# Performance work log

Measured on AMD Instinct MI355X. Metric: run time of the kernel, lower is better.

The kernel has to match this reference:

```python
import jax, jax.numpy as jnp
import numpy as np

D = 64        # state dim (num_output)
H = 256       # MLP hidden width
B = 4096      # batch
NUM_STEPS = 16  # fixed-step Dormand-Prince steps over t in [0,1] per bijector


def _mlp(t, y, W1, b1, W2, b2, W3, b3):
    # time-conditioned MLP: concat scalar t to state, two tanh layers, linear out
    tcol = jnp.full((y.shape[0], 1), t, dtype=y.dtype)
    h = jnp.tanh(jnp.concatenate([y, tcol], axis=1) @ W1 + b1)
    h = jnp.tanh(h @ W2 + b2)
    return h @ W3 + b3


def _dopri5_fixed(f, y0):
    # classic Dormand-Prince (RK45) Butcher tableau, 5th-order solution,
    # fixed step h = 1/NUM_STEPS from t=0 to t=1
    h = jnp.asarray(1.0 / NUM_STEPS, dtype=y0.dtype)

    def step(y, i):
        t = i.astype(y0.dtype) * h
        k1 = f(t, y)
        k2 = f(t + h * (1/5),  y + h * ((1/5) * k1))
        k3 = f(t + h * (3/10), y + h * ((3/40) * k1 + (9/40) * k2))
        k4 = f(t + h * (4/5),  y + h * ((44/45) * k1 - (56/15) * k2 + (32/9) * k3))
        k5 = f(t + h * (8/9),  y + h * ((19372/6561) * k1 - (25360/2187) * k2
                                        + (64448/6561) * k3 - (212/729) * k4))
        k6 = f(t + h,          y + h * ((9017/3168) * k1 - (355/33) * k2
                                        + (46732/5247) * k3 + (49/176) * k4
                                        - (5103/18656) * k5))
        y_next = y + h * ((35/384) * k1 + (500/1113) * k3 + (125/192) * k4
                          - (2187/6784) * k5 + (11/84) * k6)
        return y_next, None

    y_final, _ = jax.lax.scan(step, y0, jnp.arange(NUM_STEPS))
    return y_final


def setup_inputs() -> dict:
    key = jax.random.key(0)
    ks = jax.random.split(key, 7)
    s_in = 1.0 / np.sqrt(D + 1)
    s_h = 1.0 / np.sqrt(H)
    inp = {"x": jax.random.normal(ks[0], (B, D), dtype=jnp.float32)}
    for i, base in enumerate([1, 4]):
        inp[f"p{i}_W1"] = jax.random.normal(ks[base], (D + 1, H), dtype=jnp.float32) * s_in
        inp[f"p{i}_b1"] = jnp.zeros((H,), dtype=jnp.float32)
        inp[f"p{i}_W2"] = jax.random.normal(ks[base + 1], (H, H), dtype=jnp.float32) * s_h
        inp[f"p{i}_b2"] = jnp.zeros((H,), dtype=jnp.float32)
        inp[f"p{i}_W3"] = jax.random.normal(ks[base + 2], (H, D), dtype=jnp.float32) * s_h
        inp[f"p{i}_b3"] = jnp.zeros((D,), dtype=jnp.float32)
    return inp


def reference(x, p0_W1, p0_b1, p0_W2, p0_b2, p0_W3, p0_b3,
              p1_W1, p1_b1, p1_W2, p1_b2, p1_W3, p1_b3):
    # Chain(list(reversed(bijectors))).forward applies bijector 0 first, then 1.
    # FFJORD bijector forward = integrate dz/dt = mlp(t, z) from t=0 to t=1.
    y = x
    params = [(p0_W1, p0_b1, p0_W2, p0_b2, p0_W3, p0_b3),
              (p1_W1, p1_b1, p1_W2, p1_b2, p1_W3, p1_b3)]
    for (W1, b1, W2, b2, W3, b3) in params:
        f = lambda t, z: _mlp(t, z, W1, b1, W2, b2, W3, b3)
        y = _dopri5_fixed(f, y)
    return y
```

## Files before the change

### kernel.cpp

```cpp
#include <hip/hip_runtime.h>

typedef __attribute__((ext_vector_type(8))) short short8;
typedef __attribute__((ext_vector_type(4))) float f32x4;

#define NSTEPS 16

__device__ __forceinline__ unsigned short bf16rne(float f) {
  unsigned int u = __float_as_uint(f);
  u += 0x7FFFu + ((u >> 16) & 1u);
  return (unsigned short)(u >> 16);
}

#if __has_builtin(__builtin_amdgcn_cvt_pk_bf16_f32)
typedef __attribute__((ext_vector_type(2))) __bf16 v2bf16;
__device__ __forceinline__ unsigned int pk2(float a, float b) {
  v2bf16 t = __builtin_amdgcn_cvt_pk_bf16_f32(a, b);
  unsigned int r;
  __builtin_memcpy(&r, &t, 4);
  return r;
}
#else
__device__ __forceinline__ unsigned int pk2(float a, float b) {
  unsigned int ua = __float_as_uint(a), ub = __float_as_uint(b);
  ua += 0x7FFFu + ((ua >> 16) & 1u);
  ub += 0x7FFFu + ((ub >> 16) & 1u);
  return (ua >> 16) | (ub & 0xFFFF0000u);
}
#endif

__device__ __forceinline__ float tanh_fast(float x) {
  float e = __builtin_amdgcn_exp2f(x * 2.8853900817779268f);
  return __builtin_fmaf(-2.0f, __builtin_amdgcn_rcpf(e + 1.0f), 1.0f);
}

__global__ void ffjord_setup(const float* __restrict__ W1a, const float* __restrict__ W2a,
                             const float* __restrict__ W3a, const float* __restrict__ W1b,
                             const float* __restrict__ W2b, const float* __restrict__ W3b,
                             unsigned short* __restrict__ ws) {
  int gid = blockIdx.x * blockDim.x + threadIdx.x;
  int bij = gid / 12288;
  int r = gid - bij * 12288;
  const float* W1 = bij ? W1b : W1a;
  const float* W2 = bij ? W2b : W2a;
  const float* W3 = bij ? W3b : W3a;
  unsigned short* o = ws + bij * 98304;
  const float* src;
  int kstride;
  if (r < 2048) {
    int lane = r & 63, nt = (r >> 6) & 15, ks = r >> 10;
    int k0 = ks * 32 + (lane >> 4) * 8, n = nt * 16 + (lane & 15);
    src = W1 + k0 * 256 + n; kstride = 256; o += r * 8;
  } else if (r < 10240) {
    int rr = r - 2048;
    int lane = rr & 63, nt = (rr >> 6) & 15, ks = rr >> 10;
    int k0 = ks * 32 + (lane >> 4) * 8, n = nt * 16 + (lane & 15);
    src = W2 + k0 * 256 + n; kstride = 256; o += 16384 + rr * 8;
  } else {
    int rr = r - 10240;
    int lane = rr & 63, nt = (rr >> 6) & 3, ks = rr >> 8;
    int k0 = ks * 32 + (lane >> 4) * 8, n = nt * 16 + (lane & 15);
    src = W3 + k0 * 64 + n; kstride = 64; o += 81920 + rr * 8;
  }
  #pragma unroll
  for (int j = 0; j < 8; j++) o[j] = bf16rne(src[j * kstride]);
}

__global__ __launch_bounds__(768, 3) void ffjord_main(
    const float* __restrict__ x, float* __restrict__ out,
    const unsigned short* __restrict__ ws,
    const float* __restrict__ W1a, const float* __restrict__ b1a,
    const float* __restrict__ b2a, const float* __restrict__ b3a,
    const float* __restrict__ W1b, const float* __restrict__ b1b,
    const float* __restrict__ b2b, const float* __restrict__ b3b) {
  __shared__ __align__(16) unsigned short zA[1088];
  __shared__ __align__(16) unsigned short h1A[4096];
  __shared__ __align__(16) unsigned short h2A[4096];
  __shared__ __align__(16) unsigned short w3s[16384];
  __shared__ __align__(16) float kbuf[5][1024];

  const int tid = threadIdx.x;
  const int wave = tid >> 6;
  const int lane = tid & 63;
  const int cl = lane & 15;
  const int qd = lane >> 4;
  const int row0 = blockIdx.x * 16;

  int hoff[2];
  #pragma unroll
  for (int t = 0; t < 2; t++) {
    int c = (wave * 2 + t) * 16 + qd * 4;
    hoff[t] = (c >> 5) * 512 + ((c & 31) >> 3) * 128 + cl * 8 + (c & 7);
  }
  const int zrb = qd * 136 + cl * 8;
  const int w3i = wave & 3;
  const int dl3 = w3i * 16 + qd * 4;
  const int zw = (2 * w3i + (qd >> 1)) * 136 + cl * 8 + 4 * (qd & 1);
  const int rtid = tid - 512;

  const float hstep = 1.0f / 16.0f;

  f32x4 yc;

  const float A2[5][5] = {
      {1.f / 5.f, 0.f, 0.f, 0.f, 0.f},
      {3.f / 40.f, 9.f / 40.f, 0.f, 0.f, 0.f},
      {44.f / 45.f, -56.f / 15.f, 32.f / 9.f, 0.f, 0.f},
      {19372.f / 6561.f, -25360.f / 2187.f, 64448.f / 6561.f, -212.f / 729.f, 0.f},
      {9017.f / 3168.f, -355.f / 33.f, 46732.f / 5247.f, 49.f / 176.f, -5103.f / 18656.f}};
  const float CT[6] = {0.0f, 0.2f, 0.3f, 0.8f, 8.0f / 9.0f, 1.0f};
  const float BW0 = 35.f / 384.f, BW2 = 500.f / 1113.f, BW3 = 125.f / 192.f,
              BW4 = -2187.f / 6784.f, BW5 = 11.f / 84.f;

  for (int bij = 0; bij < 2; bij++) {
    const unsigned short* wsb = ws + bij * 98304;
    const float* W1 = bij ? W1b : W1a;
    const float* b1 = bij ? b1b : b1a;
    const float* b2 = bij ? b2b : b2a;
    const float* b3 = bij ? b3b : b3a;

    f32x4 b1c[2], w1t4[2], b2c[2];
    short8 w1f[2][2], w2f[8][2];
    f32x4 b3c;

    if (wave < 8) {
      const short8* w1p = (const short8*)wsb;
      const short8* w2p = (const short8*)(wsb + 16384);
      #pragma unroll
      for (int t = 0; t < 2; t++) {
        int c = (wave * 2 + t) * 16 + qd * 4;
        b1c[t] = *(const f32x4*)(b1 + c);
        w1t4[t] = *(const f32x4*)(W1 + 64 * 256 + c);
        b2c[t] = *(const f32x4*)(b2 + c);
        #pragma unroll
        for (int ks = 0; ks < 2; ks++)
          w1f[ks][t] = w1p[(ks * 16 + wave * 2 + t) * 64 + lane];
        #pragma unroll
        for (int ks = 0; ks < 8; ks++)
          w2f[ks][t] = w2p[(ks * 16 + wave * 2 + t) * 64 + lane];
      }
    } else {
      b3c = *(const f32x4*)(b3 + dl3);
      if (bij == 0) {
        yc = *(const f32x4*)(x + (row0 + cl) * 64 + dl3);
        uint2 pv;
        pv.x = pk2(yc[0], yc[1]);
        pv.y = pk2(yc[2], yc[3]);
        *(uint2*)(zA + zw) = pv;
      }
    }

    {
      const uint4* s4 = (const uint4*)(wsb + 81920);
      uint4* d4 = (uint4*)w3s;
      for (int i = tid; i < 2048; i += 768) d4[i] = s4[i];
    }
    __syncthreads();

    for (int step = 0; step < NSTEPS; step++) {
      float stepf = (float)step;
      #pragma unroll
      for (int s = 0; s < 6; s++) {
        float ts = (stepf + CT[s]) * hstep;

        if (wave < 8) {
          short8 a0 = *(const short8*)(zA + zrb);
          short8 a1 = *(const short8*)(zA + zrb + 544);
          #pragma unroll
          for (int t = 0; t < 2; t++) {
            f32x4 acc;
            #pragma unroll
            for (int r = 0; r < 4; r++)
              acc[r] = __builtin_fmaf(ts, w1t4[t][r], b1c[t][r]);
            acc = __builtin_amdgcn_mfma_f32_16x16x32_bf16(w1f[0][t], a0, acc, 0, 0, 0);
            acc = __builtin_amdgcn_mfma_f32_16x16x32_bf16(w1f[1][t], a1, acc, 0, 0, 0);
            uint2 pv;
            pv.x = pk2(tanh_fast(acc[0]), tanh_fast(acc[1]));
            pv.y = pk2(tanh_fast(acc[2]), tanh_fast(acc[3]));
            *(uint2*)(h1A + hoff[t]) = pv;
          }
        }
        __syncthreads();

        if (wave < 8) {
          f32x4 a0A = b2c[0], a1A = b2c[1];
          f32x4 zf; zf[0] = 0.f; zf[1] = 0.f; zf[2] = 0.f; zf[3] = 0.f;
          f32x4 a0B = zf, a1B = zf;
          #pragma unroll
          for (int ks = 0; ks < 4; ks++) {
            short8 hb = ((const short8*)h1A)[ks * 64 + lane];
            a0A = __builtin_amdgcn_mfma_f32_16x16x32_bf16(w2f[ks][0], hb, a0A, 0, 0, 0);
            a1A = __builtin_amdgcn_mfma_f32_16x16x32_bf16(w2f[ks][1], hb, a1A, 0, 0, 0);
          }
          #pragma unroll
          for (int ks = 4; ks < 8; ks++) {
            short8 hb = ((const short8*)h1A)[ks * 64 + lane];
            a0B = __builtin_amdgcn_mfma_f32_16x16x32_bf16(w2f[ks][0], hb, a0B, 0, 0, 0);
            a1B = __builtin_amdgcn_mfma_f32_16x16x32_bf16(w2f[ks][1], hb, a1B, 0, 0, 0);
          }
          uint2 pv;
          pv.x = pk2(tanh_fast(a0A[0] + a0B[0]), tanh_fast(a0A[1] + a0B[1]));
          pv.y = pk2(tanh_fast(a0A[2] + a0B[2]), tanh_fast(a0A[3] + a0B[3]));
          *(uint2*)(h2A + hoff[0]) = pv;
          pv.x = pk2(tanh_fast(a1A[0] + a1B[0]), tanh_fast(a1A[1] + a1B[1]));
          pv.y = pk2(tanh_fast(a1A[2] + a1B[2]), tanh_fast(a1A[3] + a1B[3]));
          *(uint2*)(h2A + hoff[1]) = pv;
        }
        __syncthreads();

        if (wave >= 8) {
          f32x4 accP = b3c;
          f32x4 accQ; accQ[0] = 0.f; accQ[1] = 0.f; accQ[2] = 0.f; accQ[3] = 0.f;
          #pragma unroll
          for (int ks = 0; ks < 8; ks += 2) {
            short8 hb0 = ((const short8*)h2A)[ks * 64 + lane];
            short8 wf0 = ((const short8*)w3s)[(ks * 4 + w3i) * 64 + lane];
            short8 hb1 = ((const short8*)h2A)[(ks + 1) * 64 + lane];
            short8 wf1 = ((const short8*)w3s)[((ks + 1) * 4 + w3i) * 64 + lane];
            accP = __builtin_amdgcn_mfma_f32_16x16x32_bf16(wf0, hb0, accP, 0, 0, 0);
            accQ = __builtin_amdgcn_mfma_f32_16x16x32_bf16(wf1, hb1, accQ, 0, 0, 0);
          }
          f32x4 kc;
          #pragma unroll
          for (int r = 0; r < 4; r++) kc[r] = accP[r] + accQ[r];
          if (s < 5) *(f32x4*)(&kbuf[s][rtid * 4]) = kc;

          f32x4 z;
          if (s < 5) {
            #pragma unroll
            for (int r = 0; r < 4; r++)
              z[r] = __builtin_fmaf(hstep * A2[s][s], kc[r], yc[r]);
            #pragma unroll
            for (int j = 0; j < 4; j++)
              if (j < s) {
                f32x4 kj = *(const f32x4*)(&kbuf[j][rtid * 4]);
                float a = hstep * A2[s][j];
                #pragma unroll
                for (int r = 0; r < 4; r++) z[r] = __builtin_fmaf(a, kj[r], z[r]);
              }
          } else {
            f32x4 k0 = *(const f32x4*)(&kbuf[0][rtid * 4]);
            f32x4 k2 = *(const f32x4*)(&kbuf[2][rtid * 4]);
            f32x4 k3 = *(const f32x4*)(&kbuf[3][rtid * 4]);
            f32x4 k4 = *(const f32x4*)(&kbuf[4][rtid * 4]);
            #pragma unroll
            for (int r = 0; r < 4; r++) {
              float d = BW0 * k0[r] + BW2 * k2[r] + BW3 * k3[r] +
                        BW4 * k4[r] + BW5 * kc[r];
              yc[r] += hstep * d;
              z[r] = yc[r];
            }
          }
          uint2 pv;
          pv.x = pk2(z[0], z[1]);
          pv.y = pk2(z[2], z[3]);
          *(uint2*)(zA + zw) = pv;
        }
        __syncthreads();
      }
    }
  }

  if (wave >= 8)
    *(f32x4*)(out + (row0 + cl) * 64 + dl3) = yc;
}

extern "C" void kernel_launch(void* const* d_in, const int* in_sizes, int n_in,
                              void* d_out, int out_size, void* d_ws, size_t ws_size,
                              hipStream_t stream) {
  (void)in_sizes; (void)n_in; (void)out_size; (void)ws_size;
  const float* x   = (const float*)d_in[0];
  const float* W1a = (const float*)d_in[1];
  const float* b1a = (const float*)d_in[2];
  const float* W2a = (const float*)d_in[3];
  const float* b2a = (const float*)d_in[4];
  const float* W3a = (const float*)d_in[5];
  const float* b3a = (const float*)d_in[6];
  const float* W1b = (const float*)d_in[7];
  const float* b1b = (const float*)d_in[8];
  const float* W2b = (const float*)d_in[9];
  const float* b2b = (const float*)d_in[10];
  const float* W3b = (const float*)d_in[11];
  const float* b3b = (const float*)d_in[12];
  unsigned short* ws = (unsigned short*)d_ws;
  float* out = (float*)d_out;

  hipLaunchKernelGGL(ffjord_setup, dim3(96), dim3(256), 0, stream,
                     W1a, W2a, W3a, W1b, W2b, W3b, ws);
  hipLaunchKernelGGL(ffjord_main, dim3(256), dim3(768), 0, stream,
                     x, out, ws, W1a, b1a, b2a, b3a, W1b, b1b, b2b, b3b);
}
```

Before: 343.8 us.

## Shrink blocks to 8 rows, drop dedicated W3 waves, read W3 from global

```diff
diff --git a/kernel.cpp b/kernel.cpp
--- a/kernel.cpp
+++ b/kernel.cpp
@@ -65,7 +65,7 @@
   for (int j = 0; j < 8; j++) o[j] = bf16rne(src[j * kstride]);
 }
 
-__global__ __launch_bounds__(768, 3) void ffjord_main(
+__global__ __launch_bounds__(512, 4) void ffjord_main(
     const float* __restrict__ x, float* __restrict__ out,
     const unsigned short* __restrict__ ws,
     const float* __restrict__ W1a, const float* __restrict__ b1a,
@@ -75,7 +75,6 @@
   __shared__ __align__(16) unsigned short zA[1088];
   __shared__ __align__(16) unsigned short h1A[4096];
   __shared__ __align__(16) unsigned short h2A[4096];
-  __shared__ __align__(16) unsigned short w3s[16384];
   __shared__ __align__(16) float kbuf[5][1024];
 
   const int tid = threadIdx.x;
@@ -83,7 +82,7 @@
   const int lane = tid & 63;
   const int cl = lane & 15;
   const int qd = lane >> 4;
-  const int row0 = blockIdx.x * 16;
+  const int row0 = blockIdx.x * 8;
 
   int hoff[2];
   #pragma unroll
@@ -92,10 +91,9 @@
     hoff[t] = (c >> 5) * 512 + ((c & 31) >> 3) * 128 + cl * 8 + (c & 7);
   }
   const int zrb = qd * 136 + cl * 8;
-  const int w3i = wave & 3;
-  const int dl3 = w3i * 16 + qd * 4;
-  const int zw = (2 * w3i + (qd >> 1)) * 136 + cl * 8 + 4 * (qd & 1);
-  const int rtid = tid - 512;
+  const int t3 = wave;
+  const int dl3 = t3 * 16 + qd * 4;
+  const int zw = (2 * t3 + (qd >> 1)) * 136 + cl * 8 + 4 * (qd & 1);
 
   const float hstep = 1.0f / 16.0f;
 
@@ -120,9 +118,7 @@
 
     f32x4 b1c[2], w1t4[2], b2c[2];
     short8 w1f[2][2], w2f[8][2];
-    f32x4 b3c;
-
-    if (wave < 8) {
+    {
       const short8* w1p = (const short8*)wsb;
       const short8* w2p = (const short8*)(wsb + 16384);
       #pragma unroll
@@ -138,23 +134,22 @@
         for (int ks = 0; ks < 8; ks++)
           w2f[ks][t] = w2p[(ks * 16 + wave * 2 + t) * 64 + lane];
       }
-    } else {
+    }
+    f32x4 b3c;
+    if (wave < 4) {
       b3c = *(const f32x4*)(b3 + dl3);
       if (bij == 0) {
-        yc = *(const f32x4*)(x + (row0 + cl) * 64 + dl3);
+        if (cl < 8) yc = *(const f32x4*)(x + (row0 + cl) * 64 + dl3);
+        else { yc[0] = 0.f; yc[1] = 0.f; yc[2] = 0.f; yc[3] = 0.f; }
         uint2 pv;
         pv.x = pk2(yc[0], yc[1]);
         pv.y = pk2(yc[2], yc[3]);
         *(uint2*)(zA + zw) = pv;
       }
     }
-
-    {
-      const uint4* s4 = (const uint4*)(wsb + 81920);
-      uint4* d4 = (uint4*)w3s;
-      for (int i = tid; i < 2048; i += 768) d4[i] = s4[i];
-    }
     __syncthreads();
+
+    const short8* w3p = (const short8*)(wsb + 81920);
 
     for (int step = 0; step < NSTEPS; step++) {
       float stepf = (float)step;
@@ -162,7 +157,7 @@
       for (int s = 0; s < 6; s++) {
         float ts = (stepf + CT[s]) * hstep;
 
-        if (wave < 8) {
+        {
           short8 a0 = *(const short8*)(zA + zrb);
           short8 a1 = *(const short8*)(zA + zrb + 544);
           #pragma unroll
@@ -181,7 +176,7 @@
         }
         __syncthreads();
 
-        if (wave < 8) {
+        {
           f32x4 a0A = b2c[0], a1A = b2c[1];
           f32x4 zf; zf[0] = 0.f; zf[1] = 0.f; zf[2] = 0.f; zf[3] = 0.f;
           f32x4 a0B = zf, a1B = zf;
@@ -207,22 +202,22 @@
         }
         __syncthreads();
 
-        if (wave >= 8) {
+        if (wave < 4) {
           f32x4 accP = b3c;
           f32x4 accQ; accQ[0] = 0.f; accQ[1] = 0.f; accQ[2] = 0.f; accQ[3] = 0.f;
           #pragma unroll
           for (int ks = 0; ks < 8; ks += 2) {
             short8 hb0 = ((const short8*)h2A)[ks * 64 + lane];
-            short8 wf0 = ((const short8*)w3s)[(ks * 4 + w3i) * 64 + lane];
+            short8 wf0 = w3p[(ks * 4 + t3) * 64 + lane];
             short8 hb1 = ((const short8*)h2A)[(ks + 1) * 64 + lane];
-            short8 wf1 = ((const short8*)w3s)[((ks + 1) * 4 + w3i) * 64 + lane];
+            short8 wf1 = w3p[((ks + 1) * 4 + t3) * 64 + lane];
             accP = __builtin_amdgcn_mfma_f32_16x16x32_bf16(wf0, hb0, accP, 0, 0, 0);
             accQ = __builtin_amdgcn_mfma_f32_16x16x32_bf16(wf1, hb1, accQ, 0, 0, 0);
           }
           f32x4 kc;
           #pragma unroll
           for (int r = 0; r < 4; r++) kc[r] = accP[r] + accQ[r];
-          if (s < 5) *(f32x4*)(&kbuf[s][rtid * 4]) = kc;
+          if (s < 5) *(f32x4*)(&kbuf[s][tid * 4]) = kc;
 
           f32x4 z;
           if (s < 5) {
@@ -232,16 +227,16 @@
             #pragma unroll
             for (int j = 0; j < 4; j++)
               if (j < s) {
-                f32x4 kj = *(const f32x4*)(&kbuf[j][rtid * 4]);
+                f32x4 kj = *(const f32x4*)(&kbuf[j][tid * 4]);
                 float a = hstep * A2[s][j];
                 #pragma unroll
                 for (int r = 0; r < 4; r++) z[r] = __builtin_fmaf(a, kj[r], z[r]);
               }
           } else {
-            f32x4 k0 = *(const f32x4*)(&kbuf[0][rtid * 4]);
-            f32x4 k2 = *(const f32x4*)(&kbuf[2][rtid * 4]);
-            f32x4 k3 = *(const f32x4*)(&kbuf[3][rtid * 4]);
-            f32x4 k4 = *(const f32x4*)(&kbuf[4][rtid * 4]);
+            f32x4 k0 = *(const f32x4*)(&kbuf[0][tid * 4]);
+            f32x4 k2 = *(const f32x4*)(&kbuf[2][tid * 4]);
+            f32x4 k3 = *(const f32x4*)(&kbuf[3][tid * 4]);
+            f32x4 k4 = *(const f32x4*)(&kbuf[4][tid * 4]);
             #pragma unroll
             for (int r = 0; r < 4; r++) {
               float d = BW0 * k0[r] + BW2 * k2[r] + BW3 * k3[r] +
@@ -260,7 +255,7 @@
     }
   }
 
-  if (wave >= 8)
+  if (wave < 4 && cl < 8)
     *(f32x4*)(out + (row0 + cl) * 64 + dl3) = yc;
 }
 
@@ -286,6 +281,6 @@
 
   hipLaunchKernelGGL(ffjord_setup, dim3(96), dim3(256), 0, stream,
                      W1a, W2a, W3a, W1b, W2b, W3b, ws);
-  hipLaunchKernelGGL(ffjord_main, dim3(256), dim3(768), 0, stream,
+  hipLaunchKernelGGL(ffjord_main, dim3(512), dim3(512), 0, stream,
                      x, out, ws, W1a, b1a, b2a, b3a, W1b, b1b, b2b, b3b);
 }
```

After: 1.110 ms. +222.8%, slower.
